# Performance work log

Hardware: AMD Instinct MI355X
Metric: run time of the kernel (lower is better)

Reference implementation:

```python
import jax, jax.numpy as jnp
import numpy as np
import math

B, H, S, D = 4, 16, 4096, 128

def setup_inputs() -> dict:
    key = jax.random.key(0)
    kq, kk, kv = jax.random.split(key, 3)
    q = jax.random.normal(kq, (B, H, S, D), dtype=jnp.float32)
    k = jax.random.normal(kk, (B, H, S, D), dtype=jnp.float32)
    v = jax.random.normal(kv, (B, H, S, D), dtype=jnp.float32)
    return {"q": q, "k": k, "v": v}

def reference(q, k, v):
    # Faithful to the torch module: score = (q^T @ k) / sqrt(n_heads)
    # q^T contracts over the SEQUENCE axis -> (B, H, D, D) feature-attention.
    n_heads = q.shape[1]
    scale = 1.0 / math.sqrt(n_heads)
    score = jnp.einsum('bhsd,bhse->bhde', q, k) * scale  # (B,H,D,D)
    score = jax.nn.softmax(score, axis=-1)
    # score @ v^T -> (B,H,D,S)
    out = jnp.einsum('bhde,bhse->bhds', score, v)
    return out
```

## Files before the change

kernel.cpp:

```cpp
#include <hip/hip_runtime.h>

#define BH 64
#define S_ 4096
#define D_ 128
#define SCALE 0.25f

typedef __attribute__((ext_vector_type(4))) short short4v;
typedef __attribute__((ext_vector_type(8))) short short8v;
typedef __attribute__((ext_vector_type(4))) float f32x4;

__device__ inline unsigned short f2bf(float x) {
  union { float f; unsigned u; } v; v.f = x;
  unsigned r = v.u + 0x7fff + ((v.u >> 16) & 1);
  return (unsigned short)(r >> 16);
}
__device__ inline short8v cat8(short4v a, short4v b) {
  short8v r;
  r[0] = a[0]; r[1] = a[1]; r[2] = a[2]; r[3] = a[3];
  r[4] = b[0]; r[5] = b[1]; r[6] = b[2]; r[7] = b[3];
  return r;
}
__device__ inline short4v tr16(unsigned addr) {
  short4v r;
  asm volatile("ds_read_b64_tr_b16 %0, %1" : "=v"(r) : "v"(addr));
  return r;
}
__device__ inline void cvt_pair(float x0, float x1, unsigned& hi, unsigned& lo) {
  unsigned u0 = __float_as_uint(x0), u1 = __float_as_uint(x1);
  unsigned m0 = u0 & 0xffff0000u, m1 = u1 & 0xffff0000u;
  hi = m1 | (u0 >> 16);
  float l0 = x0 - __uint_as_float(m0);
  float l1 = x1 - __uint_as_float(m1);
  lo = (__float_as_uint(l1) & 0xffff0000u) | (__float_as_uint(l0) >> 16);
}

#define TILE_B2 8192
#define TILE_U2 2048
#define TILE_SH2 4096
#define BUF_B2  (4 * TILE_B2)
#define BUF_SH2 (4 * TILE_SH2)

template <int NKS, bool ATOMIC>
__global__ __launch_bounds__(512, 2) void qk_mfma(const float* __restrict__ q,
                                                  const float* __restrict__ k,
                                                  float* __restrict__ part) {
  constexpr int schunk = S_ / NKS;
  constexpr int nsteps = schunk / 32;
  static_assert(nsteps % 2 == 0, "nsteps must be even (buffer pairing)");
  const int bh = blockIdx.x;
  const int ks = blockIdx.y;
  const float* qb = q + (size_t)bh * S_ * D_ + (size_t)ks * schunk * D_;
  const float* kb = k + (size_t)bh * S_ * D_ + (size_t)ks * schunk * D_;

  __shared__ alignas(16) short lds[2 * BUF_SH2];
  unsigned* ldsU0 = (unsigned*)&lds[0];
  unsigned* ldsU1 = (unsigned*)&lds[BUF_SH2];
  const unsigned base_u = (unsigned)(uintptr_t)&lds[0];

  const int tid = threadIdx.x;
  const int wv = tid >> 6, lane = tid & 63;
  const int wm = wv & 3;
  const int wn = wv >> 2;

  f32x4 acc[2][4];
#pragma unroll
  for (int a = 0; a < 2; ++a)
#pragma unroll
    for (int b = 0; b < 4; ++b) acc[a][b] = (f32x4){0.f, 0.f, 0.f, 0.f};

  const unsigned lconst = ((unsigned)(lane >> 4) << 10) |
                          ((unsigned)((lane & 15) >> 2) << 5) |
                          ((unsigned)(lane & 3) << 3);
  const unsigned trbase = base_u + lconst;
  const unsigned aQ0 = trbase;
  const unsigned aK0 = trbase + 2u * TILE_B2;
  const unsigned aQ1 = aQ0 + BUF_B2;
  const unsigned aK1 = aK0 + BUF_B2;

  const int row0 = ((tid >> 7) << 2) | ((tid >> 2) & 3);
  const int col0 = (((tid >> 4) & 7) << 4) | ((tid & 3) << 2);

  float4 qr[2], kr[2];
  auto load_step = [&](int st) {
    size_t o0 = (size_t)(st * 32 + row0) * D_ + col0;
    size_t o1 = o0 + (size_t)16 * D_;
    qr[0] = *(const float4*)(qb + o0);
    qr[1] = *(const float4*)(qb + o1);
    kr[0] = *(const float4*)(kb + o0);
    kr[1] = *(const float4*)(kb + o1);
  };
  auto cvt_store = [&](unsigned* bufU) {
#pragma unroll
    for (int i = 0; i < 2; ++i) {
      unsigned off = (unsigned)(tid + i * 512) * 2;
      unsigned h0, l0, h1, l1;
      cvt_pair(qr[i].x, qr[i].y, h0, l0);
      cvt_pair(qr[i].z, qr[i].w, h1, l1);
      *(uint2*)(bufU + off) = make_uint2(h0, h1);
      *(uint2*)(bufU + TILE_U2 + off) = make_uint2(l0, l1);
      cvt_pair(kr[i].x, kr[i].y, h0, l0);
      cvt_pair(kr[i].z, kr[i].w, h1, l1);
      *(uint2*)(bufU + 2 * TILE_U2 + off) = make_uint2(h0, h1);
      *(uint2*)(bufU + 3 * TILE_U2 + off) = make_uint2(l0, l1);
    }
  };

  auto iter = [&](int st, unsigned aQb, unsigned aKb, unsigned* stageU) {
    short4v Bf[4][2][2];
#pragma unroll
    for (int b = 0; b < 4; ++b) {
      unsigned cb = (unsigned)(wn * 4 + b) << 7;
#pragma unroll
      for (int ver = 0; ver < 2; ++ver)
#pragma unroll
        for (int kh = 0; kh < 2; ++kh)
          Bf[b][ver][kh] = tr16(aKb + ver * TILE_B2 + kh * 4096 + cb);
    }
    short4v Af[2][2][2];
#pragma unroll
    for (int a = 0; a < 2; ++a) {
      unsigned cb = (unsigned)(wm * 2 + a) << 7;
#pragma unroll
      for (int ver = 0; ver < 2; ++ver)
#pragma unroll
        for (int kh = 0; kh < 2; ++kh)
          Af[a][ver][kh] = tr16(aQb + ver * TILE_B2 + kh * 4096 + cb);
    }
    if (st + 1 < nsteps) cvt_store(stageU);
    if (st + 2 < nsteps) load_step(st + 2);
    asm volatile("s_waitcnt lgkmcnt(0)" ::: "memory");
    __builtin_amdgcn_sched_barrier(0);
#pragma unroll
    for (int a = 0; a < 2; ++a) {
      short8v ah = cat8(Af[a][0][0], Af[a][0][1]);
      short8v al = cat8(Af[a][1][0], Af[a][1][1]);
#pragma unroll
      for (int b = 0; b < 4; ++b) {
        short8v bh_ = cat8(Bf[b][0][0], Bf[b][0][1]);
        short8v bl_ = cat8(Bf[b][1][0], Bf[b][1][1]);
        acc[a][b] = __builtin_amdgcn_mfma_f32_16x16x32_bf16(ah, bh_, acc[a][b], 0, 0, 0);
        acc[a][b] = __builtin_amdgcn_mfma_f32_16x16x32_bf16(ah, bl_, acc[a][b], 0, 0, 0);
        acc[a][b] = __builtin_amdgcn_mfma_f32_16x16x32_bf16(al, bh_, acc[a][b], 0, 0, 0);
      }
    }
    __builtin_amdgcn_s_barrier();
  };

  load_step(0);
  cvt_store(ldsU0);
  if (nsteps > 1) load_step(1);
  asm volatile("s_waitcnt lgkmcnt(0)" ::: "memory");
  __builtin_amdgcn_s_barrier();

  for (int st = 0; st < nsteps; st += 2) {
    iter(st, aQ0, aK0, ldsU1);
    iter(st + 1, aQ1, aK1, ldsU0);
  }

  if (!ATOMIC) {
    float* dst = part + ((size_t)ks * BH + bh) * D_ * D_;
#pragma unroll
    for (int a = 0; a < 2; ++a)
#pragma unroll
      for (int b = 0; b < 4; ++b) {
        int e = (wn * 4 + b) * 16 + (lane & 15);
#pragma unroll
        for (int r = 0; r < 4; ++r) {
          int d = (wm * 2 + a) * 16 + ((lane >> 4) << 2) + r;
          dst[(size_t)d * D_ + e] = acc[a][b][r] * SCALE;
        }
      }
  } else {
    float* dst = part + (size_t)bh * D_ * D_;
#pragma unroll
    for (int a = 0; a < 2; ++a)
#pragma unroll
      for (int b = 0; b < 4; ++b) {
        int e = (wn * 4 + b) * 16 + (lane & 15);
#pragma unroll
        for (int r = 0; r < 4; ++r) {
          int d = (wm * 2 + a) * 16 + ((lane >> 4) << 2) + r;
          atomicAdd(&dst[(size_t)d * D_ + e], acc[a][b][r] * SCALE);
        }
      }
  }
}

template <int NKS>
__global__ __launch_bounds__(256) void softmax_k(const float* __restrict__ part,
                                                 short* __restrict__ Pg) {
  const int bh = blockIdx.x;
  const int wv = threadIdx.x >> 6, lane = threadIdx.x & 63;
  const size_t kstride = (size_t)BH * D_ * D_;
  const float* base = part + (size_t)bh * D_ * D_;
  short* dst = Pg + (size_t)bh * D_ * D_;
#pragma unroll
  for (int i = 0; i < 8; ++i) {
    int d = blockIdx.y * 32 + wv * 8 + i;
    float v0 = 0.f, v1 = 0.f;
    for (int ks2 = 0; ks2 < NKS; ++ks2) {
      const float* row = base + ks2 * kstride + (size_t)d * D_;
      v0 += row[lane];
      v1 += row[lane + 64];
    }
    float m = fmaxf(v0, v1);
#pragma unroll
    for (int off = 32; off; off >>= 1) m = fmaxf(m, __shfl_xor(m, off, 64));
    float e0 = __expf(v0 - m), e1 = __expf(v1 - m);
    float s = e0 + e1;
#pragma unroll
    for (int off = 32; off; off >>= 1) s += __shfl_xor(s, off, 64);
    float inv = 1.f / s;
    dst[(size_t)d * D_ + lane] = (short)f2bf(e0 * inv);
    dst[(size_t)d * D_ + lane + 64] = (short)f2bf(e1 * inv);
  }
}

__global__ __launch_bounds__(256) void pv_mfma(const short* __restrict__ Pg,
                                               const float* __restrict__ v,
                                               float* __restrict__ out) {
  const int bh = blockIdx.x;
  const int s0 = blockIdx.y * 128;
  const float* vb = v + (size_t)bh * S_ * D_;
  __shared__ alignas(16) short P_lds[128 * 136];
  __shared__ alignas(16) short V_lds[128 * 36];
  const int tid = threadIdx.x;
  const int wv = tid >> 6, lane = tid & 63;

  const short* Pb = Pg + (size_t)bh * D_ * D_;
#pragma unroll
  for (int i = 0; i < 8; ++i) {
    int idx8 = tid + i * 256;
    int row = idx8 >> 4, c8 = idx8 & 15;
    short8v val = *(const short8v*)(Pb + row * 128 + c8 * 8);
    *(short8v*)(P_lds + row * 136 + c8 * 8) = val;
  }

  f32x4 acc[8][2];
#pragma unroll
  for (int i = 0; i < 8; ++i)
#pragma unroll
    for (int j = 0; j < 2; ++j) acc[i][j] = (f32x4){0.f, 0.f, 0.f, 0.f};

#pragma unroll
  for (int es = 0; es < 4; ++es) {
    __syncthreads();
#pragma unroll
    for (int i = 0; i < 4; ++i) {
      int idx4 = tid + i * 256;
      int s = idx4 >> 3, c4 = idx4 & 7;
      float4 x = *(const float4*)(vb + (size_t)(s0 + s) * D_ + es * 32 + c4 * 4);
      short4v h;
      h[0] = (short)f2bf(x.x); h[1] = (short)f2bf(x.y);
      h[2] = (short)f2bf(x.z); h[3] = (short)f2bf(x.w);
      *(short4v*)(V_lds + s * 36 + c4 * 4) = h;
    }
    __syncthreads();

    short8v a[8];
#pragma unroll
    for (int mt = 0; mt < 8; ++mt) {
      int d = mt * 16 + (lane & 15);
      const short* pr = P_lds + d * 136 + es * 32 + ((lane >> 4) << 2);
      a[mt] = cat8(*(const short4v*)pr, *(const short4v*)(pr + 16));
    }
#pragma unroll
    for (int nl = 0; nl < 2; ++nl) {
      int srow = (wv * 2 + nl) * 16 + (lane & 15);
      const short* vr = V_lds + srow * 36 + ((lane >> 4) << 2);
      short8v b = cat8(*(const short4v*)vr, *(const short4v*)(vr + 16));
#pragma unroll
      for (int mt = 0; mt < 8; ++mt)
        acc[mt][nl] = __builtin_amdgcn_mfma_f32_16x16x32_bf16(a[mt], b, acc[mt][nl], 0, 0, 0);
    }
  }

  float* ob = out + (size_t)bh * D_ * S_ + s0;
#pragma unroll
  for (int mt = 0; mt < 8; ++mt)
#pragma unroll
    for (int nl = 0; nl < 2; ++nl) {
      int sc = (wv * 2 + nl) * 16 + (lane & 15);
#pragma unroll
      for (int r = 0; r < 4; ++r) {
        int d = mt * 16 + ((lane >> 4) << 2) + r;
        ob[(size_t)d * S_ + sc] = acc[mt][nl][r];
      }
    }
}

extern "C" void kernel_launch(void* const* d_in, const int* in_sizes, int n_in,
                              void* d_out, int out_size, void* d_ws,
                              size_t ws_size, hipStream_t stream) {
  const float* q = (const float*)d_in[0];
  const float* k = (const float*)d_in[1];
  const float* v = (const float*)d_in[2];
  float* out = (float*)d_out;
  char* ws = (char*)d_ws;

  const size_t PART1 = (size_t)BH * D_ * D_ * sizeof(float);
  const size_t PSZ = (size_t)BH * D_ * D_ * sizeof(short);

  if (ws_size >= 8 * PART1 + PSZ) {
    float* part = (float*)ws;
    short* Pg = (short*)(ws + 8 * PART1);
    qk_mfma<8, false><<<dim3(BH, 8), 512, 0, stream>>>(q, k, part);
    softmax_k<8><<<dim3(BH, 4), 256, 0, stream>>>(part, Pg);
    pv_mfma<<<dim3(BH, 32), 256, 0, stream>>>(Pg, v, out);
  } else {
    float* part = (float*)ws;
    short* Pg = (short*)(ws + PART1);
    hipMemsetAsync(ws, 0, PART1, stream);
    qk_mfma<16, true><<<dim3(BH, 16), 512, 0, stream>>>(q, k, part);
    softmax_k<1><<<dim3(BH, 4), 256, 0, stream>>>(part, Pg);
    pv_mfma<<<dim3(BH, 32), 256, 0, stream>>>(Pg, v, out);
  }
}
```

Baseline: 149.0 us.

## Stage Q/K fp32 tiles via async global-to-LDS DMA with single bf16 buffer

Replaces register-staged global loads with global_load_lds async copies of fp32 Q/K tiles into a dedicated LDS staging area. Threads then read the fp32 tile from LDS, split it into hi/lo bf16 and write it into a single (no longer double-buffered) bf16 buffer. This is meant to free VGPRs and let the DMA overlap the MFMA work. In exchange it adds an extra barrier per step plus extra LDS reads, and the bf16 buffer is single-buffered, so conversion must wait for the operand reads to finish.

New measurement: 153.4 us. +2.9%, slower.

```diff
diff --git a/kernel.cpp b/kernel.cpp
--- a/kernel.cpp
+++ b/kernel.cpp
@@ -33,12 +33,17 @@
   float l1 = x1 - __uint_as_float(m1);
   lo = (__float_as_uint(l1) & 0xffff0000u) | (__float_as_uint(l0) >> 16);
 }
+__device__ __forceinline__ void async_copy16(void* lds_dst, const void* g_src) {
+  __builtin_amdgcn_global_load_lds(
+      (const __attribute__((address_space(1))) void*)g_src,
+      (__attribute__((address_space(3))) void*)lds_dst, 16, 0, 0);
+}
 
 #define TILE_B2 8192
 #define TILE_U2 2048
 #define TILE_SH2 4096
-#define BUF_B2  (4 * TILE_B2)
-#define BUF_SH2 (4 * TILE_SH2)
+#define F_SH 16384
+#define F_ROW_F 128
 
 template <int NKS, bool ATOMIC>
 __global__ __launch_bounds__(512, 2) void qk_mfma(const float* __restrict__ q,
@@ -46,16 +51,16 @@
                                                   float* __restrict__ part) {
   constexpr int schunk = S_ / NKS;
   constexpr int nsteps = schunk / 32;
-  static_assert(nsteps % 2 == 0, "nsteps must be even (buffer pairing)");
   const int bh = blockIdx.x;
   const int ks = blockIdx.y;
   const float* qb = q + (size_t)bh * S_ * D_ + (size_t)ks * schunk * D_;
   const float* kb = k + (size_t)bh * S_ * D_ + (size_t)ks * schunk * D_;
 
-  __shared__ alignas(16) short lds[2 * BUF_SH2];
-  unsigned* ldsU0 = (unsigned*)&lds[0];
-  unsigned* ldsU1 = (unsigned*)&lds[BUF_SH2];
+  __shared__ alignas(16) short lds[F_SH + 2 * 8192];
+  unsigned* bufU = (unsigned*)&lds[0];
   const unsigned base_u = (unsigned)(uintptr_t)&lds[0];
+  float* FQ = (float*)&lds[F_SH];
+  float* FK = (float*)&lds[F_SH + 8192];
 
   const int tid = threadIdx.x;
   const int wv = tid >> 6, lane = tid & 63;
@@ -72,40 +77,64 @@
                           ((unsigned)((lane & 15) >> 2) << 5) |
                           ((unsigned)(lane & 3) << 3);
   const unsigned trbase = base_u + lconst;
-  const unsigned aQ0 = trbase;
-  const unsigned aK0 = trbase + 2u * TILE_B2;
-  const unsigned aQ1 = aQ0 + BUF_B2;
-  const unsigned aK1 = aK0 + BUF_B2;
+  const unsigned aQ = trbase;
+  const unsigned aK = trbase + 2u * TILE_B2;
 
   const int row0 = ((tid >> 7) << 2) | ((tid >> 2) & 3);
   const int col0 = (((tid >> 4) & 7) << 4) | ((tid & 3) << 2);
 
-  float4 qr[2], kr[2];
-  auto load_step = [&](int st) {
-    size_t o0 = (size_t)(st * 32 + row0) * D_ + col0;
-    size_t o1 = o0 + (size_t)16 * D_;
-    qr[0] = *(const float4*)(qb + o0);
-    qr[1] = *(const float4*)(qb + o1);
-    kr[0] = *(const float4*)(kb + o0);
-    kr[1] = *(const float4*)(kb + o1);
+  const int mK = wv >> 2;
+  const int w4 = wv & 3;
+  const float* matp = mK ? kb : qb;
+  short* ldsF = &lds[F_SH + mK * 8192];
+
+  auto dma_step = [&](int st) {
+#pragma unroll
+    for (int i = 0; i < 4; ++i) {
+      const float* src =
+          matp + (size_t)(st * 32 + w4 * 8 + i * 2 + (lane >> 5)) * D_ +
+          (lane & 31) * 4;
+      async_copy16(ldsF + (size_t)(w4 * 4 + i) * 512, src);
+    }
   };
-  auto cvt_store = [&](unsigned* bufU) {
+
+  float4 freg[4];
+  auto f_read = [&]() {
+    freg[0] = *(const float4*)(FQ + row0 * F_ROW_F + col0);
+    freg[1] = *(const float4*)(FQ + (row0 + 16) * F_ROW_F + col0);
+    freg[2] = *(const float4*)(FK + row0 * F_ROW_F + col0);
+    freg[3] = *(const float4*)(FK + (row0 + 16) * F_ROW_F + col0);
+  };
+  auto cvt_store = [&]() {
 #pragma unroll
     for (int i = 0; i < 2; ++i) {
       unsigned off = (unsigned)(tid + i * 512) * 2;
       unsigned h0, l0, h1, l1;
-      cvt_pair(qr[i].x, qr[i].y, h0, l0);
-      cvt_pair(qr[i].z, qr[i].w, h1, l1);
+      cvt_pair(freg[i].x, freg[i].y, h0, l0);
+      cvt_pair(freg[i].z, freg[i].w, h1, l1);
       *(uint2*)(bufU + off) = make_uint2(h0, h1);
       *(uint2*)(bufU + TILE_U2 + off) = make_uint2(l0, l1);
-      cvt_pair(kr[i].x, kr[i].y, h0, l0);
-      cvt_pair(kr[i].z, kr[i].w, h1, l1);
+      cvt_pair(freg[i + 2].x, freg[i + 2].y, h0, l0);
+      cvt_pair(freg[i + 2].z, freg[i + 2].w, h1, l1);
       *(uint2*)(bufU + 2 * TILE_U2 + off) = make_uint2(h0, h1);
       *(uint2*)(bufU + 3 * TILE_U2 + off) = make_uint2(l0, l1);
     }
   };
 
-  auto iter = [&](int st, unsigned aQb, unsigned aKb, unsigned* stageU) {
+  dma_step(0);
+  asm volatile("s_waitcnt vmcnt(0)" ::: "memory");
+  __builtin_amdgcn_s_barrier();
+  f_read();
+  asm volatile("s_waitcnt lgkmcnt(0)" ::: "memory");
+  __builtin_amdgcn_sched_barrier(0);
+  __builtin_amdgcn_s_barrier();
+  if (nsteps > 1) dma_step(1);
+  cvt_store();
+  asm volatile("s_waitcnt vmcnt(0) lgkmcnt(0)" ::: "memory");
+  __builtin_amdgcn_sched_barrier(0);
+  __builtin_amdgcn_s_barrier();
+
+  for (int st = 0; st < nsteps; ++st) {
     short4v Bf[4][2][2];
 #pragma unroll
     for (int b = 0; b < 4; ++b) {
@@ -114,7 +143,7 @@
       for (int ver = 0; ver < 2; ++ver)
 #pragma unroll
         for (int kh = 0; kh < 2; ++kh)
-          Bf[b][ver][kh] = tr16(aKb + ver * TILE_B2 + kh * 4096 + cb);
+          Bf[b][ver][kh] = tr16(aK + ver * TILE_B2 + kh * 4096 + cb);
     }
     short4v Af[2][2][2];
 #pragma unroll
@@ -124,12 +153,16 @@
       for (int ver = 0; ver < 2; ++ver)
 #pragma unroll
         for (int kh = 0; kh < 2; ++kh)
-          Af[a][ver][kh] = tr16(aQb + ver * TILE_B2 + kh * 4096 + cb);
-    }
-    if (st + 1 < nsteps) cvt_store(stageU);
-    if (st + 2 < nsteps) load_step(st + 2);
+          Af[a][ver][kh] = tr16(aQ + ver * TILE_B2 + kh * 4096 + cb);
+    }
+    if (st + 1 < nsteps) f_read();
     asm volatile("s_waitcnt lgkmcnt(0)" ::: "memory");
     __builtin_amdgcn_sched_barrier(0);
+    __builtin_amdgcn_s_barrier();
+
+    if (st + 2 < nsteps) dma_step(st + 2);
+    if (st + 1 < nsteps) cvt_store();
+
 #pragma unroll
     for (int a = 0; a < 2; ++a) {
       short8v ah = cat8(Af[a][0][0], Af[a][0][1]);
@@ -143,18 +176,9 @@
         acc[a][b] = __builtin_amdgcn_mfma_f32_16x16x32_bf16(al, bh_, acc[a][b], 0, 0, 0);
       }
     }
+    asm volatile("s_waitcnt vmcnt(0) lgkmcnt(0)" ::: "memory");
+    __builtin_amdgcn_sched_barrier(0);
     __builtin_amdgcn_s_barrier();
-  };
-
-  load_step(0);
-  cvt_store(ldsU0);
-  if (nsteps > 1) load_step(1);
-  asm volatile("s_waitcnt lgkmcnt(0)" ::: "memory");
-  __builtin_amdgcn_s_barrier();
-
-  for (int st = 0; st < nsteps; st += 2) {
-    iter(st, aQ0, aK0, ldsU1);
-    iter(st + 1, aQ1, aK1, ldsU0);
   }
 
   if (!ATOMIC) {
```
